# Performance work log

Hardware: AMD Instinct MI355X
Metric: run time of the kernel (lower is better)

Reference implementation:

```python
import jax, jax.numpy as jnp
import numpy as np

D_MODEL = 256
NHEAD = 8
AGG = 4
NPE = (832.0, 832.0, 832.0, 832.0)
LAYER_NAMES = ['self', 'cross'] * 4


def layer_norm(x, g, b, eps=1e-5):
    mu = x.mean(-1, keepdims=True)
    var = ((x - mu) ** 2).mean(-1, keepdims=True)
    return (x - mu) * jax.lax.rsqrt(var + eps) * g + b


def rope_tables(h, w, d_model=D_MODEL):
    # i/j positions start at 1 (torch cumsum of ones); npe train/test scaling
    i = (jnp.arange(1, h + 1, dtype=jnp.float32) * (NPE[0] / NPE[2]))[:, None, None]
    j = (jnp.arange(1, w + 1, dtype=jnp.float32) * (NPE[1] / NPE[3]))[None, :, None]
    d4 = d_model // 4
    div = jnp.exp(jnp.arange(d4, dtype=jnp.float32) * (-np.log(10000.0) / d4))

    def interleave(a, bb):
        a = jnp.broadcast_to(a, (h, w, d4))
        bb = jnp.broadcast_to(bb, (h, w, d4))
        return jnp.stack([a, bb], -1).reshape(h, w, 2 * d4)

    sin = interleave(jnp.sin(i * div), jnp.sin(j * div))
    cos = interleave(jnp.cos(i * div), jnp.cos(j * div))
    return jnp.repeat(sin, 2, axis=-1), jnp.repeat(cos, 2, axis=-1)  # [h,w,d_model]


def rotate_half(x):
    xp = x.reshape(*x.shape[:-1], -1, 2)
    return jnp.stack([-xp[..., 1], xp[..., 0]], -1).reshape(*x.shape)


def apply_rope(x, sin, cos):  # x: [b,h,w,c]
    return x * cos + rotate_half(x) * sin


def encoder_layer(x, source, p, use_rope):
    bs, C, H0, W0 = x.shape
    # depthwise-conv aggregation of query features (stride=kernel=AGG, no bias)
    q = jax.lax.conv_general_dilated(
        x, p['agg_w'], (AGG, AGG), 'VALID',
        dimension_numbers=('NCHW', 'OIHW', 'NCHW'), feature_group_count=C)
    q = layer_norm(q.transpose(0, 2, 3, 1), p['ln1_g'], p['ln1_b'])  # [b,h,w,C]
    # max-pool aggregation of source features
    s = jax.lax.reduce_window(source, -jnp.inf, jax.lax.max,
                              (1, 1, AGG, AGG), (1, 1, AGG, AGG), 'VALID')
    s = layer_norm(s.transpose(0, 2, 3, 1), p['ln1_g'], p['ln1_b'])
    query = q @ p['qw']
    key = s @ p['kw']
    value = s @ p['vw']
    if use_rope:
        sin_q, cos_q = rope_tables(query.shape[1], query.shape[2])
        query = apply_rope(query, sin_q, cos_q)
        sin_k, cos_k = rope_tables(key.shape[1], key.shape[2])
        key = apply_rope(key, sin_k, cos_k)
    L = query.shape[1] * query.shape[2]
    S = key.shape[1] * key.shape[2]
    dh = C // NHEAD
    qh = query.reshape(bs, L, NHEAD, dh)
    kh = key.reshape(bs, S, NHEAD, dh)
    vh = value.reshape(bs, S, NHEAD, dh)
    scores = jnp.einsum('blhd,bshd->bhls', qh, kh) / jnp.asarray(dh, qh.dtype) ** 0.5
    attn = jax.nn.softmax(scores, axis=-1)
    m = jnp.einsum('bhls,bshd->blhd', attn, vh).reshape(bs, L, C)
    m = m @ p['mw']  # merge
    m = m.reshape(bs, H0 // AGG, W0 // AGG, C).transpose(0, 3, 1, 2)
    # bilinear upsample x4, align_corners=False (half-pixel, matches jax.image)
    m = jax.image.resize(m, (bs, C, H0, W0), method='bilinear')
    cat = jnp.concatenate([x, m], axis=1).transpose(0, 2, 3, 1)  # [b,H,W,2C]
    h1 = cat @ p['w1']
    h1 = jnp.where(h1 >= 0, h1, 0.01 * h1)  # LeakyReLU
    out = layer_norm(h1 @ p['w2'], p['ln2_g'], p['ln2_b']).transpose(0, 3, 1, 2)
    return x + out


def _forward(feat0, feat1, params):
    for i, name in enumerate(LAYER_NAMES):
        p = {k: v[i] for k, v in params.items()}
        if name == 'self':
            feat0 = encoder_layer(feat0, feat0, p, use_rope=True)
            feat1 = encoder_layer(feat1, feat1, p, use_rope=True)
        else:
            feat0 = encoder_layer(feat0, feat1, p, use_rope=False)
            feat1 = encoder_layer(feat1, feat0, p, use_rope=False)
    return feat0, feat1


def setup_inputs() -> dict:
    key = jax.random.key(0)
    ks = jax.random.split(key, 10)
    C = D_MODEL
    NL = len(LAYER_NAMES)

    def xavier(k, shape, fan_in, fan_out):
        return jax.random.normal(k, shape, jnp.float32) * np.sqrt(2.0 / (fan_in + fan_out))

    return {
        'feat0': jax.random.normal(ks[0], (2, C, 96, 96), jnp.float32),
        'feat1': jax.random.normal(ks[1], (2, C, 96, 96), jnp.float32),
        'agg_w': jax.random.normal(ks[2], (NL, C, 1, AGG, AGG), jnp.float32) * 0.1,
        'qw': xavier(ks[3], (NL, C, C), C, C),
        'kw': xavier(ks[4], (NL, C, C), C, C),
        'vw': xavier(ks[5], (NL, C, C), C, C),
        'mw': xavier(ks[6], (NL, C, C), C, C),
        'w1': xavier(ks[7], (NL, 2 * C, 2 * C), 2 * C, 2 * C),
        'w2': xavier(ks[8], (NL, 2 * C, C), 2 * C, C),
        'ln1_g': jnp.ones((NL, C), jnp.float32),
        'ln1_b': jnp.zeros((NL, C), jnp.float32),
        'ln2_g': jnp.ones((NL, C), jnp.float32),
        'ln2_b': jnp.zeros((NL, C), jnp.float32),
    }


def reference(feat0, feat1, agg_w, qw, kw, vw, mw, w1, w2, ln1_g, ln1_b, ln2_g, ln2_b):
    params = dict(agg_w=agg_w, qw=qw, kw=kw, vw=vw, mw=mw, w1=w1, w2=w2,
                  ln1_g=ln1_g, ln1_b=ln1_b, ln2_g=ln2_g, ln2_b=ln2_b)
    return _forward(feat0, feat1, params)
```

## Files before the change

kernel.cpp:

```cpp
#include <hip/hip_runtime.h>
#include <math.h>

constexpr int BSZ = 2;
constexpr int CH  = 256;
constexpr int IH  = 96, IW = 96;
constexpr int HSS = 24, WSS = 24;
constexpr int SL  = HSS * WSS;
constexpr int NHD = 8, DHD = 32;
constexpr int CH2 = 512;
constexpr int PIX = IH * IW;
constexpr int MFFN = BSZ * PIX;
constexpr long FEATN = (long)BSZ * PIX * CH;

typedef __attribute__((ext_vector_type(4))) float f32x4;
typedef _Float16 f16;
typedef __attribute__((ext_vector_type(8))) _Float16 f16x8;
typedef __attribute__((ext_vector_type(4))) _Float16 f16x4;


__device__ inline void gload16(const void* g, void* l) {
  __builtin_amdgcn_global_load_lds(
      (const __attribute__((address_space(1))) unsigned int*)g,
      (__attribute__((address_space(3))) unsigned int*)l, 16, 0, 0);
}

__global__ __launch_bounds__(256) void k_in_tr(const float* __restrict__ in,
                                               f16* __restrict__ outh) {
  __shared__ float t[32][33];
  const int b = blockIdx.z;
  const int p0 = blockIdx.x * 32, c0 = blockIdx.y * 32;
  const int tx = threadIdx.x & 31, ty = threadIdx.x >> 5;
#pragma unroll
  for (int r = 0; r < 4; ++r)
    t[tx][ty + r * 8] = in[((long)b * CH + c0 + ty + r * 8) * PIX + p0 + tx];
  __syncthreads();
#pragma unroll
  for (int r = 0; r < 4; ++r) {
    long row = (long)b * PIX + p0 + ty + r * 8;
    outh[row * CH + ((c0 + tx) ^ (ty << 3))] = (f16)t[ty + r * 8][tx];
  }
}

__global__ __launch_bounds__(256) void k_out_tr(const f16* __restrict__ in,
                                                float* __restrict__ out) {
  __shared__ float t[32][33];
  const int b = blockIdx.z;
  const int p0 = blockIdx.x * 32, c0 = blockIdx.y * 32;
  const int tx = threadIdx.x & 31, ty = threadIdx.x >> 5;
#pragma unroll
  for (int r = 0; r < 4; ++r)
    t[ty + r * 8][tx] =
        (float)in[((long)b * PIX + p0 + ty + r * 8) * CH + ((c0 + tx) ^ (ty << 3))];
  __syncthreads();
#pragma unroll
  for (int r = 0; r < 4; ++r)
    out[((long)b * CH + c0 + ty + r * 8) * PIX + p0 + tx] = t[tx][ty + r * 8];
}

__global__ __launch_bounds__(256) void k_wt(const float* __restrict__ W,
                                            f16* __restrict__ WT,
                                            int K, int N, long strideW, long strideT) {
  const long z = blockIdx.z;
  W  += z * strideW;
  WT += z * strideT;
  __shared__ float t[32][33];
  const int n0 = blockIdx.x * 32, k0 = blockIdx.y * 32;
  const int tx = threadIdx.x & 31, ty = threadIdx.x >> 5;
#pragma unroll
  for (int r = 0; r < 4; ++r)
    t[ty + r * 8][tx] = W[(long)(k0 + ty + r * 8) * N + n0 + tx];
  __syncthreads();
#pragma unroll
  for (int r = 0; r < 4; ++r) {
    int n = n0 + ty + r * 8;
    WT[(long)n * K + ((k0 + tx) ^ ((n & 7) << 3))] = (f16)t[tx][ty + r * 8];
  }
}

__global__ __launch_bounds__(256) void k_cvt(const float* __restrict__ W,
                                             f16* __restrict__ O) {
  const int i = blockIdx.x;
  const long z = blockIdx.y;
  const int k = threadIdx.x;
  O[(z * CH + i) * CH + (k ^ ((i & 7) << 3))] = (f16)W[(z * CH + i) * CH + k];
}

__global__ __launch_bounds__(256) void k_rope_tables(float* __restrict__ sinT,
                                                     float* __restrict__ cosT) {
  int l = blockIdx.x;
  int d = threadIdx.x;
  int ii = l / WSS + 1;
  int jj = l % WSS + 1;
  int kidx = d >> 2;
  bool is_i = ((d >> 1) & 1) == 0;
  float div = expf((float)kidx * -0.14391156831212787f);
  float pos = is_i ? (float)ii : (float)jj;
  float ang = pos * div;
  sinT[(long)l * CH + d] = sinf(ang);
  cosT[(long)l * CH + d] = cosf(ang);
}

__global__ __launch_bounds__(64) void k_agg(const f16* __restrict__ x,
                                            const f16* __restrict__ src,
                                            const float* __restrict__ aggw,
                                            const float* __restrict__ g,
                                            const float* __restrict__ bt,
                                            f16* __restrict__ qln,
                                            f16* __restrict__ sln,
                                            int nb, int same) {
  int bi = blockIdx.x;
  int mode = 0;
  const int nblk = nb * SL / 2;
  if (!same && bi >= nblk) { mode = 1; bi -= nblk; }
  const int doConv = same || (mode == 0);
  const int doPool = same || (mode == 1);
  const int tid = threadIdx.x;
  const int tok = tid >> 5, cg = tid & 31;
  const int lg = bi * 2 + tok;
  const int b = lg / SL, l = lg - b * SL;
  const int i = l / WSS, j = l - i * WSS;
  const f16* in = mode ? src : x;

  float cv[8] = {};
  float mv[8];
#pragma unroll
  for (int e = 0; e < 8; ++e) mv[e] = -INFINITY;
#pragma unroll
  for (int r = 0; r < 4; ++r)
#pragma unroll
    for (int s = 0; s < 4; ++s) {
      const int px = j * 4 + s;
      f16x8 v = *(const f16x8*)&in[(((size_t)b * IH + i * 4 + r) * IW + px) * CH +
                                   ((cg * 8) ^ ((px & 7) << 3))];
#pragma unroll
      for (int e = 0; e < 8; ++e) {
        float f = (float)v[e];
        cv[e] += f * aggw[(cg * 8 + e) * 16 + r * 4 + s];
        mv[e] = fmaxf(mv[e], f);
      }
    }
  const size_t orow = (size_t)(b * SL + l) * CH + ((cg * 8) ^ ((l & 7) << 3));
  if (doConv) {
    float s1 = 0.f, s2 = 0.f;
#pragma unroll
    for (int e = 0; e < 8; ++e) { s1 += cv[e]; s2 += cv[e] * cv[e]; }
#pragma unroll
    for (int d = 1; d < 32; d <<= 1) { s1 += __shfl_xor(s1, d); s2 += __shfl_xor(s2, d); }
    float mu = s1 * (1.f / CH);
    float var = s2 * (1.f / CH) - mu * mu;
    float rs = rsqrtf(var + 1e-5f);
    f16x8 o;
#pragma unroll
    for (int e = 0; e < 8; ++e)
      o[e] = (f16)((cv[e] - mu) * rs * g[cg * 8 + e] + bt[cg * 8 + e]);
    *(f16x8*)&qln[orow] = o;
  }
  if (doPool) {
    float s1 = 0.f, s2 = 0.f;
#pragma unroll
    for (int e = 0; e < 8; ++e) { s1 += mv[e]; s2 += mv[e] * mv[e]; }
#pragma unroll
    for (int d = 1; d < 32; d <<= 1) { s1 += __shfl_xor(s1, d); s2 += __shfl_xor(s2, d); }
    float mu = s1 * (1.f / CH);
    float var = s2 * (1.f / CH) - mu * mu;
    float rs = rsqrtf(var + 1e-5f);
    f16x8 o;
#pragma unroll
    for (int e = 0; e < 8; ++e)
      o[e] = (f16)((mv[e] - mu) * rs * g[cg * 8 + e] + bt[cg * 8 + e]);
    *(f16x8*)&sln[orow] = o;
  }
}

template <int BM, int BN, int OUT>
__global__ __launch_bounds__(256) void k_mm(const f16* __restrict__ A,
                                            const f16* __restrict__ A2,
                                            const f16* __restrict__ Bt,
                                            void* __restrict__ C0, void* __restrict__ C1,
                                            void* __restrict__ C2,
                                            int M, int K, int lda, int ldb,
                                            int koffA, int koffB, int ldc,
                                            const float* __restrict__ sinT,
                                            const float* __restrict__ cosT,
                                            long zsA, long zsB, long zsC) {
  constexpr int BK = 64;
  constexpr int WM = BM / 2, WN = BN / 2;
  constexpr int FM = WM / 16, FN = WN / 16;
  constexpr int RA = BM * BK / 2048, RB = BN * BK / 2048;
  __shared__ f16 As[2][BM * BK];
  __shared__ f16 Bs[2][BN * BK];
  const int tid = threadIdx.x;
  const int lane = tid & 63, w = tid >> 6;
  const int wr = w >> 1, wc = w & 1;
  const int lq = lane & 15, g = lane >> 4;
  const int sw = (lq & 7) << 3;
  const int bm = blockIdx.x * BM, bn = blockIdx.y * BN;
  const long z = blockIdx.z;
  const f16* Ap = ((OUT == 4 && bn >= CH) ? A2 : A) + z * zsA + koffA;
  const f16* Bp = Bt + z * zsB + koffB;

  auto stA = [&](int buf, int k0) {
#pragma unroll
    for (int i = 0; i < RA; ++i) {
      int e = (i * 256 + tid) * 8;
      gload16(Ap + (size_t)(bm + (e >> 6)) * lda + k0 + (e & 63), &As[buf][e]);
    }
  };
  auto stB = [&](int buf, int k0) {
#pragma unroll
    for (int i = 0; i < RB; ++i) {
      int e = (i * 256 + tid) * 8;
      gload16(Bp + (size_t)(bn + (e >> 6)) * ldb + k0 + (e & 63), &Bs[buf][e]);
    }
  };

  f32x4 acc[FM][FN] = {};
  stA(0, 0); stB(0, 0);
  asm volatile("s_waitcnt vmcnt(0)" ::: "memory");
  __syncthreads();
  int cur = 0;
  for (int k0 = 0; k0 < K; k0 += BK) {
    if (k0 + BK < K) { stA(cur ^ 1, k0 + BK); stB(cur ^ 1, k0 + BK); }
#pragma unroll
    for (int ks = 0; ks < 2; ++ks) {
      const int kx = (ks * 32 + g * 8) ^ sw;
      f16x8 a[FM], b[FN];
#pragma unroll
      for (int m = 0; m < FM; ++m)
        a[m] = *(const f16x8*)&As[cur][(wr * WM + m * 16 + lq) * BK + kx];
#pragma unroll
      for (int n = 0; n < FN; ++n)
        b[n] = *(const f16x8*)&Bs[cur][(wc * WN + n * 16 + lq) * BK + kx];
#pragma unroll
      for (int m = 0; m < FM; ++m)
#pragma unroll
        for (int n = 0; n < FN; ++n)
          acc[m][n] = __builtin_amdgcn_mfma_f32_16x16x32_f16(a[m], b[n], acc[m][n], 0, 0, 0);
    }
    __syncthreads();
    cur ^= 1;
  }
#pragma unroll
  for (int m = 0; m < FM; ++m) {
    const int rowb = bm + wr * WM + m * 16 + g * 4;
#pragma unroll
    for (int n = 0; n < FN; ++n) {
      const int col = bn + wc * WN + n * 16 + lq;
#pragma unroll
      for (int r = 0; r < 4; ++r) {
        const int row = rowb + r;
        float v = acc[m][n][r];
        if (OUT == 0) {
          ((float*)C0 + z * zsC)[(size_t)row * ldc + col] = v;
        } else if (OUT == 5) {
          ((f16*)C0 + z * zsC)[(size_t)row * ldc + (col ^ ((row & 7) << 3))] = (f16)v;
        } else {
          const int b = row / SL, s = row - b * SL;
          const int which = col >> 8;
          const int ch = col & 255;
          float vp = __shfl_xor(v, 1);
          if (which < 2 && sinT) {
            float sn = sinT[(size_t)s * CH + ch];
            float cs = cosT[(size_t)s * CH + ch];
            v = ((lane & 1) == 0) ? v * cs - vp * sn : v * cs + vp * sn;
          }
          if (which == 0) v *= 0.17677669529663687f;
          const int h = ch >> 5, d = ch & 31;
          if (which == 0)
            ((f16*)C0)[(((size_t)b * NHD + h) * SL + s) * DHD + d] = (f16)v;
          else if (which == 1)
            ((f16*)C1)[(((size_t)b * NHD + h) * SL + s) * DHD + d] = (f16)v;
          else
            ((f16*)C2)[(((size_t)b * NHD + h) * DHD + d) * SL + s] = (f16)v;
        }
      }
    }
  }
}

__global__ __launch_bounds__(128) void k_attn(const f16* __restrict__ qh,
                                              const f16* __restrict__ kh,
                                              const f16* __restrict__ vt,
                                              f16* __restrict__ msgA) {
  const int bh = blockIdx.x;
  const int b = bh >> 3, h = bh & 7;
  const int tid = threadIdx.x;
  const int sid = tid >> 6;
  const int lane = tid & 63;
  const int lq = lane & 15, g = lane >> 4;
  const int q0 = blockIdx.y * 16;

  const f16x8 qf = *(const f16x8*)&qh[((size_t)bh * SL + q0 + lq) * DHD + g * 8];
  const f16* kbase = kh + (size_t)bh * SL * DHD;
  const f16* vbase = vt + (size_t)bh * DHD * SL;
  const int t0 = sid * 18;

  f16x8 kf = *(const f16x8*)&kbase[((size_t)(t0 * 16 + lq)) * DHD + g * 8];
  f16x4 va = *(const f16x4*)&vbase[(size_t)lq * SL + t0 * 16 + g * 4];
  f16x4 vb = *(const f16x4*)&vbase[(size_t)(16 + lq) * SL + t0 * 16 + g * 4];

  f32x4 o0 = {}, o1 = {};
  float m = -1e30f, l = 0.f;
  for (int tt = 0; tt < 18; ++tt) {
    const int t = t0 + tt;
    const int tn = tt < 17 ? t + 1 : t;
    f16x8 kfn = *(const f16x8*)&kbase[((size_t)(tn * 16 + lq)) * DHD + g * 8];
    f16x4 van = *(const f16x4*)&vbase[(size_t)lq * SL + tn * 16 + g * 4];
    f16x4 vbn = *(const f16x4*)&vbase[(size_t)(16 + lq) * SL + tn * 16 + g * 4];
    f32x4 s = __builtin_amdgcn_mfma_f32_16x16x32_f16(kf, qf, (f32x4){0.f, 0.f, 0.f, 0.f}, 0, 0, 0);
    float tm = fmaxf(fmaxf(s[0], s[1]), fmaxf(s[2], s[3]));
    tm = fmaxf(tm, __shfl_xor(tm, 16));
    tm = fmaxf(tm, __shfl_xor(tm, 32));
    if (__any(tm > m + 5.f)) {
      float mn = fmaxf(m, tm);
      float f = __expf(m - mn);
      o0 *= f; o1 *= f; l *= f; m = mn;
    }
    float e0 = __expf(s[0] - m), e1 = __expf(s[1] - m);
    float e2 = __expf(s[2] - m), e3 = __expf(s[3] - m);
    l += (e0 + e1) + (e2 + e3);
    f16x4 ef = {(f16)e0, (f16)e1, (f16)e2, (f16)e3};
    o0 = __builtin_amdgcn_mfma_f32_16x16x16f16(va, ef, o0, 0, 0, 0);
    o1 = __builtin_amdgcn_mfma_f32_16x16x16f16(vb, ef, o1, 0, 0, 0);
    kf = kfn; va = van; vb = vbn;
  }
  l += __shfl_xor(l, 16);
  l += __shfl_xor(l, 32);

  __shared__ float mS[2][16], lS[2][16];
  __shared__ float oS[2][2][16][17];
  if (g == 0) { mS[sid][lq] = m; lS[sid][lq] = l; }
#pragma unroll
  for (int r = 0; r < 4; ++r) {
    oS[sid][0][g * 4 + r][lq] = o0[r];
    oS[sid][1][g * 4 + r][lq] = o1[r];
  }
  __syncthreads();
  float m0 = mS[0][lq], m1 = mS[1][lq];
  float l0 = lS[0][lq], l1 = lS[1][lq];
  float mn = fmaxf(m0, m1);
  float f0 = __expf(m0 - mn), f1 = __expf(m1 - mn);
  float inv = 1.f / (l0 * f0 + l1 * f1);
  f16x4 ov;
#pragma unroll
  for (int r = 0; r < 4; ++r)
    ov[r] = (f16)((oS[0][sid][g * 4 + r][lq] * f0 + oS[1][sid][g * 4 + r][lq] * f1) * inv);
  const int swz = (lq & 7) << 3;
  f16* mrow = msgA + ((size_t)(b * SL + q0 + lq)) * CH;
  *(f16x4*)&mrow[(h * DHD + sid * 16 + g * 4) ^ swz] = ov;
}

__global__ __launch_bounds__(512) void k_ffn1(const f16* __restrict__ xh,
                                              const f16* __restrict__ w1T,
                                              const float* __restrict__ Z,
                                              f16* __restrict__ h1) {
  constexpr int BM = 128, BN = 128, BK = 64, K = 256;
  constexpr int WM = 32, WN = 64, FM = 2, FN = 4;
  __shared__ f16 As[2][BM * BK];
  __shared__ f16 Bs[BN * BK];
  const int tid = threadIdx.x;
  const int lane = tid & 63, w = tid >> 6;
  const int wr = w >> 1, wc = w & 1;
  const int lq = lane & 15, g = lane >> 4;
  const int sw = (lq & 7) << 3;
  const int bm = blockIdx.x * BM, bn = blockIdx.y * BN;

  auto stA = [&](int buf, int k0) {
#pragma unroll
    for (int i = 0; i < 2; ++i) {
      int e = (i * 512 + tid) * 8;
      gload16(xh + (size_t)(bm + (e >> 6)) * 256 + k0 + (e & 63), &As[buf][e]);
    }
  };
  auto stB = [&](int k0) {
#pragma unroll
    for (int i = 0; i < 2; ++i) {
      int e = (i * 512 + tid) * 8;
      gload16(w1T + (size_t)(bn + (e >> 6)) * 512 + k0 + (e & 63), &Bs[e]);
    }
  };

  f32x4 acc[FM][FN] = {};
  stA(0, 0); stB(0);
  asm volatile("s_waitcnt vmcnt(0)" ::: "memory");
  __syncthreads();
  int cur = 0;
  for (int k0 = 0; k0 < K; k0 += BK) {
    if (k0 + BK < K) stA(cur ^ 1, k0 + BK);
#pragma unroll
    for (int ks = 0; ks < 2; ++ks) {
      const int kx = (ks * 32 + g * 8) ^ sw;
      f16x8 a[FM], b[FN];
#pragma unroll
      for (int m = 0; m < FM; ++m)
        a[m] = *(const f16x8*)&As[cur][(wr * WM + m * 16 + lq) * BK + kx];
#pragma unroll
      for (int n = 0; n < FN; ++n)
        b[n] = *(const f16x8*)&Bs[(wc * WN + n * 16 + lq) * BK + kx];
#pragma unroll
      for (int m = 0; m < FM; ++m)
#pragma unroll
        for (int n = 0; n < FN; ++n)
          acc[m][n] = __builtin_amdgcn_mfma_f32_16x16x32_f16(a[m], b[n], acc[m][n], 0, 0, 0);
    }
    __syncthreads();
    if (k0 + BK < K) stB(k0 + BK);
    asm volatile("s_waitcnt vmcnt(0)" ::: "memory");
    __syncthreads();
    cur ^= 1;
  }
#pragma unroll
  for (int m = 0; m < FM; ++m) {
    const int rowb = bm + wr * WM + m * 16 + g * 4;
#pragma unroll
    for (int r = 0; r < 4; ++r) {
      const int row = rowb + r;
      const int b = row / PIX;
      const int p = row - b * PIX;
      const int y = p / IW, xx = p - y * IW;
      float sy = (y + 0.5f) * 0.25f - 0.5f;
      float sx = (xx + 0.5f) * 0.25f - 0.5f;
      int y0 = (int)floorf(sy); float wy = sy - y0;
      int x0 = (int)floorf(sx); float wx = sx - x0;
      int y1 = min(y0 + 1, HSS - 1); y0 = max(y0, 0);
      int x1 = min(x0 + 1, WSS - 1); x0 = max(x0, 0);
      const float* Zb = Z + (size_t)b * SL * CH2;
      const float* z00 = Zb + (size_t)(y0 * WSS + x0) * CH2;
      const float* z01 = Zb + (size_t)(y0 * WSS + x1) * CH2;
      const float* z10 = Zb + (size_t)(y1 * WSS + x0) * CH2;
      const float* z11 = Zb + (size_t)(y1 * WSS + x1) * CH2;
      float w00 = (1.f - wy) * (1.f - wx), w01 = (1.f - wy) * wx;
      float w10 = wy * (1.f - wx), w11 = wy * wx;
      const int rs = (row & 7) << 3;
#pragma unroll
      for (int n = 0; n < FN; ++n) {
        const int col = bn + wc * WN + n * 16 + lq;
        float v = acc[m][n][r] + w00 * z00[col] + w01 * z01[col] +
                  w10 * z10[col] + w11 * z11[col];
        v = v >= 0.f ? v : 0.01f * v;
        h1[(size_t)row * CH2 + (col ^ rs)] = (f16)v;
      }
    }
  }
}

__global__ __launch_bounds__(512) void k_ffn2(const f16* __restrict__ A,
                                              const f16* __restrict__ Bt,
                                              const float* __restrict__ g2,
                                              const float* __restrict__ b2,
                                              f16* __restrict__ xh) {
  constexpr int BM = 64, BK = 64, K = 512;
  __shared__ f16 As[2][BM * BK];
  __shared__ f16 Bs[256 * BK];
  __shared__ float sS[2][BM], sQ[2][BM];
  __shared__ float gS[256], bS[256];
  const int tid = threadIdx.x;
  const int lane = tid & 63, w = tid >> 6;
  const int wr = w >> 1, wc = w & 1;
  const int lq = lane & 15, g = lane >> 4;
  const int sw = (lq & 7) << 3;
  const int bm = blockIdx.x * BM;
  if (tid < 256) { gS[tid] = g2[tid]; bS[tid] = b2[tid]; }

  auto stA = [&](int buf, int k0) {
    int e = tid * 8;
    gload16(A + (size_t)(bm + (e >> 6)) * K + k0 + (e & 63), &As[buf][e]);
  };
  auto stB = [&](int k0) {
#pragma unroll
    for (int i = 0; i < 4; ++i) {
      int e = (i * 512 + tid) * 8;
      gload16(Bt + (size_t)(e >> 6) * K + k0 + (e & 63), &Bs[e]);
    }
  };

  f32x4 acc[8] = {};
  stA(0, 0); stB(0);
  asm volatile("s_waitcnt vmcnt(0)" ::: "memory");
  __syncthreads();
  int cur = 0;
  for (int k0 = 0; k0 < K; k0 += BK) {
    if (k0 + BK < K) stA(cur ^ 1, k0 + BK);
#pragma unroll
    for (int ks = 0; ks < 2; ++ks) {
      const int kx = (ks * 32 + g * 8) ^ sw;
      f16x8 a = *(const f16x8*)&As[cur][(wr * 16 + lq) * BK + kx];
      f16x8 b[8];
#pragma unroll
      for (int n = 0; n < 8; ++n)
        b[n] = *(const f16x8*)&Bs[(wc * 128 + n * 16 + lq) * BK + kx];
#pragma unroll
      for (int n = 0; n < 8; ++n)
        acc[n] = __builtin_amdgcn_mfma_f32_16x16x32_f16(a, b[n], acc[n], 0, 0, 0);
    }
    __syncthreads();
    if (k0 + BK < K) stB(k0 + BK);
    asm volatile("s_waitcnt vmcnt(0)" ::: "memory");
    __syncthreads();
    cur ^= 1;
  }
#pragma unroll
  for (int r = 0; r < 4; ++r) {
    float s1 = 0.f, s2 = 0.f;
#pragma unroll
    for (int n = 0; n < 8; ++n) {
      float v = acc[n][r];
      s1 += v; s2 += v * v;
    }
#pragma unroll
    for (int d = 1; d < 16; d <<= 1) {
      s1 += __shfl_xor(s1, d);
      s2 += __shfl_xor(s2, d);
    }
    if (lq == 0) {
      int row = wr * 16 + g * 4 + r;
      sS[wc][row] = s1; sQ[wc][row] = s2;
    }
  }
  __syncthreads();
#pragma unroll
  for (int r = 0; r < 4; ++r) {
    int row = wr * 16 + g * 4 + r;
    float mu = (sS[0][row] + sS[1][row]) * (1.f / CH);
    float var = (sQ[0][row] + sQ[1][row]) * (1.f / CH) - mu * mu;
    float rs = rsqrtf(var + 1e-5f);
    f16* base = xh + (size_t)(bm + row) * CH;
    const int swr = ((bm + row) & 7) << 3;
#pragma unroll
    for (int n = 0; n < 8; ++n) {
      int col = wc * 128 + n * 16 + lq;
      float o = (acc[n][r] - mu) * rs * gS[col] + bS[col];
      int ci = col ^ swr;
      base[ci] = (f16)((float)base[ci] + o);
    }
  }
}

struct LayerP {
  const float *aggw, *g1, *b1, *g2, *b2;
  const f16 *qkvT, *w1T, *w2T, *wcT;
};

struct Bufs {
  f16 *qln, *sln, *msgA, *h1, *xh;
  f16 *qh, *kh, *vt;
  float *Zbuf;
  const float *sinT, *cosT;
};

static void attn_part(long xoff, long soff, const LayerP& p, bool rope, int nb,
                      const Bufs& B, hipStream_t stream) {
  const int M = nb * SL;
  const int same = (xoff == soff) ? 1 : 0;
  const int nblk = (same ? 1 : 2) * nb * SL / 2;
  k_agg<<<dim3(nblk), 64, 0, stream>>>(B.xh + xoff, B.xh + soff, p.aggw,
                                       p.g1, p.b1, B.qln, B.sln, nb, same);
  const float* sT = rope ? B.sinT : nullptr;
  const float* cT = rope ? B.cosT : nullptr;
  k_mm<32, 64, 4><<<dim3(M / 32, 12), 256, 0, stream>>>(
      B.qln, B.sln, p.qkvT, B.qh, B.kh, B.vt, M, CH, CH, CH, 0, 0, 0, sT, cT, 0, 0, 0);
  k_attn<<<dim3(nb * NHD, 36), 128, 0, stream>>>(B.qh, B.kh, B.vt, B.msgA);
  k_mm<64, 64, 0><<<dim3(M / 64, 8), 256, 0, stream>>>(
      B.msgA, nullptr, p.wcT, B.Zbuf, nullptr, nullptr, M, CH, CH, CH, 0, 0, CH2,
      nullptr, nullptr, 0, 0, 0);
}

static void ffn_part(int fi, int nf, const float* Zs, const LayerP& p, const Bufs& B,
                     hipStream_t stream) {
  const int M = nf * MFFN;
  k_ffn1<<<dim3(M / 128, CH2 / 128), 512, 0, stream>>>(B.xh + (long)fi * FEATN, p.w1T, Zs, B.h1);
  k_ffn2<<<dim3(M / 64), 512, 0, stream>>>(B.h1, p.w2T, p.g2, p.b2,
                                           B.xh + (long)fi * FEATN);
}

extern "C" void kernel_launch(void* const* d_in, const int* in_sizes, int n_in,
                              void* d_out, int out_size, void* d_ws, size_t ws_size,
                              hipStream_t stream) {
  const float* in_f0 = (const float*)d_in[0];
  const float* in_f1 = (const float*)d_in[1];
  const float* aggw  = (const float*)d_in[2];
  const float* qw    = (const float*)d_in[3];
  const float* kw    = (const float*)d_in[4];
  const float* vw    = (const float*)d_in[5];
  const float* mw    = (const float*)d_in[6];
  const float* w1    = (const float*)d_in[7];
  const float* w2    = (const float*)d_in[8];
  const float* g1    = (const float*)d_in[9];
  const float* b1    = (const float*)d_in[10];
  const float* g2    = (const float*)d_in[11];
  const float* b2    = (const float*)d_in[12];
  (void)in_sizes; (void)n_in; (void)out_size; (void)ws_size;

  char* cur = (char*)d_ws;
  auto alloc = [&](size_t bytes) { void* p = cur; cur += (bytes + 255) & ~(size_t)255; return p; };
  f16*   xh   = (f16*)alloc((size_t)2 * FEATN * 2);
  f16*   h1   = (f16*)alloc((size_t)2 * MFFN * CH2 * 2);
  float* Zbuf = (float*)alloc((size_t)4 * SL * CH2 * 4);
  f16*   msgA = (f16*)alloc((size_t)4 * SL * CH * 2);
  f16*   qln  = (f16*)alloc((size_t)4 * SL * CH * 2);
  f16*   sln  = (f16*)alloc((size_t)4 * SL * CH * 2);
  f16* qh = (f16*)alloc((size_t)4 * NHD * SL * DHD * 2);
  f16* kh = (f16*)alloc((size_t)4 * NHD * SL * DHD * 2);
  f16* vt = (f16*)alloc((size_t)4 * NHD * SL * DHD * 2);
  float* sinT = (float*)alloc((size_t)SL * CH * 4);
  float* cosT = (float*)alloc((size_t)SL * CH * 4);
  f16* qkvT = (f16*)alloc((size_t)8 * 3 * CH * CH * 2);
  f16* mwH  = (f16*)alloc((size_t)8 * CH * CH * 2);
  f16* w1T  = (f16*)alloc((size_t)8 * CH2 * CH2 * 2);
  f16* w2T  = (f16*)alloc((size_t)8 * CH * CH2 * 2);
  f16* wcT  = (f16*)alloc((size_t)8 * CH2 * CH * 2);

  k_in_tr<<<dim3(PIX / 32, CH / 32, BSZ), 256, 0, stream>>>(in_f0, xh);
  k_in_tr<<<dim3(PIX / 32, CH / 32, BSZ), 256, 0, stream>>>(in_f1, xh + FEATN);
  k_rope_tables<<<dim3(SL), 256, 0, stream>>>(sinT, cosT);
  k_wt<<<dim3(CH / 32, CH / 32, 8), 256, 0, stream>>>(qw, qkvT, CH, CH, (long)CH * CH, (long)3 * CH * CH);
  k_wt<<<dim3(CH / 32, CH / 32, 8), 256, 0, stream>>>(kw, qkvT + (size_t)CH * CH, CH, CH, (long)CH * CH, (long)3 * CH * CH);
  k_wt<<<dim3(CH / 32, CH / 32, 8), 256, 0, stream>>>(vw, qkvT + (size_t)2 * CH * CH, CH, CH, (long)CH * CH, (long)3 * CH * CH);
  k_cvt<<<dim3(CH, 8), 256, 0, stream>>>(mw, mwH);
  k_wt<<<dim3(CH2 / 32, CH2 / 32, 8), 256, 0, stream>>>(w1, w1T, CH2, CH2, (long)CH2 * CH2, (long)CH2 * CH2);
  k_wt<<<dim3(CH / 32, CH2 / 32, 8), 256, 0, stream>>>(w2, w2T, CH2, CH, (long)CH2 * CH, (long)CH * CH2);
  k_mm<64, 64, 5><<<dim3(CH2 / 64, CH / 64, 8), 256, 0, stream>>>(
      w1T, nullptr, mwH, wcT, nullptr, nullptr, CH2, CH, CH2, CH, 256, 0, CH,
      nullptr, nullptr, (long)CH2 * CH2, (long)CH * CH, (long)CH2 * CH);

  Bufs B{qln, sln, msgA, h1, xh, qh, kh, vt, Zbuf, sinT, cosT};

  for (int i = 0; i < 8; ++i) {
    LayerP p{aggw + (long)i * CH * 16,
             g1 + i * CH, b1 + i * CH, g2 + i * CH, b2 + i * CH,
             qkvT + (long)i * 3 * CH * CH,
             w1T + (long)i * CH2 * CH2, w2T + (long)i * CH * CH2,
             wcT + (long)i * CH2 * CH};
    if ((i & 1) == 0) {
      attn_part(0, 0, p, true, 4, B, stream);
      ffn_part(0, 2, Zbuf, p, B, stream);
    } else {
      attn_part(0, FEATN, p, false, 2, B, stream);
      ffn_part(0, 1, Zbuf, p, B, stream);
      attn_part(FEATN, 0, p, false, 2, B, stream);
      ffn_part(1, 1, Zbuf, p, B, stream);
    }
  }

  float* outp = (float*)d_out;
  k_out_tr<<<dim3(PIX / 32, CH / 32, BSZ), 256, 0, stream>>>(xh, outp);
  k_out_tr<<<dim3(PIX / 32, CH / 32, BSZ), 256, 0, stream>>>(xh + FEATN, outp + FEATN);
}
```

Baseline: 975.4 us.

## Split FFN2 into a 128x128-tiled GEMM plus a separate LayerNorm-residual kernel

The second FFN GEMM previously used a 64-row tile covering all 256 output columns so it could fuse LayerNorm and the residual add. It now reuses a templated 128x128 GEMM shared with FFN1, writing an fp16 intermediate h2, and a new lightweight kernel does the LayerNorm and residual update. The message-projection output Z is also stored in fp16 instead of fp32, halving its traffic and its reads in the FFN1 bilinear epilogue. In exchange, the fused epilogue becomes an extra launch plus an h2 write and read, and Z loses precision.

```diff
diff --git a/kernel.cpp b/kernel.cpp
--- a/kernel.cpp
+++ b/kernel.cpp
@@ -254,6 +254,8 @@
           ((float*)C0 + z * zsC)[(size_t)row * ldc + col] = v;
         } else if (OUT == 5) {
           ((f16*)C0 + z * zsC)[(size_t)row * ldc + (col ^ ((row & 7) << 3))] = (f16)v;
+        } else if (OUT == 6) {
+          ((f16*)C0 + z * zsC)[(size_t)row * ldc + col] = (f16)v;
         } else {
           const int b = row / SL, s = row - b * SL;
           const int which = col >> 8;
@@ -350,11 +352,13 @@
   *(f16x4*)&mrow[(h * DHD + sid * 16 + g * 4) ^ swz] = ov;
 }
 
-__global__ __launch_bounds__(512) void k_ffn1(const f16* __restrict__ xh,
-                                              const f16* __restrict__ w1T,
-                                              const float* __restrict__ Z,
-                                              f16* __restrict__ h1) {
-  constexpr int BM = 128, BN = 128, BK = 64, K = 256;
+template <int K, bool ZEPI>
+__global__ __launch_bounds__(512) void k_ffn(const f16* __restrict__ A,
+                                             const f16* __restrict__ Bt,
+                                             const f16* __restrict__ Z,
+                                             f16* __restrict__ C,
+                                             int lda, int ldc) {
+  constexpr int BM = 128, BN = 128, BK = 64;
   constexpr int WM = 32, WN = 64, FM = 2, FN = 4;
   __shared__ f16 As[2][BM * BK];
   __shared__ f16 Bs[BN * BK];
@@ -369,14 +373,14 @@
 #pragma unroll
     for (int i = 0; i < 2; ++i) {
       int e = (i * 512 + tid) * 8;
-      gload16(xh + (size_t)(bm + (e >> 6)) * 256 + k0 + (e & 63), &As[buf][e]);
+      gload16(A + (size_t)(bm + (e >> 6)) * lda + k0 + (e & 63), &As[buf][e]);
     }
   };
   auto stB = [&](int k0) {
 #pragma unroll
     for (int i = 0; i < 2; ++i) {
       int e = (i * 512 + tid) * 8;
-      gload16(w1T + (size_t)(bn + (e >> 6)) * 512 + k0 + (e & 63), &Bs[e]);
+      gload16(Bt + (size_t)(bn + (e >> 6)) * 512 + k0 + (e & 63), &Bs[e]);
     }
   };
 
@@ -415,125 +419,71 @@
 #pragma unroll
     for (int r = 0; r < 4; ++r) {
       const int row = rowb + r;
-      const int b = row / PIX;
-      const int p = row - b * PIX;
-      const int y = p / IW, xx = p - y * IW;
-      float sy = (y + 0.5f) * 0.25f - 0.5f;
-      float sx = (xx + 0.5f) * 0.25f - 0.5f;
-      int y0 = (int)floorf(sy); float wy = sy - y0;
-      int x0 = (int)floorf(sx); float wx = sx - x0;
-      int y1 = min(y0 + 1, HSS - 1); y0 = max(y0, 0);
-      int x1 = min(x0 + 1, WSS - 1); x0 = max(x0, 0);
-      const float* Zb = Z + (size_t)b * SL * CH2;
-      const float* z00 = Zb + (size_t)(y0 * WSS + x0) * CH2;
-      const float* z01 = Zb + (size_t)(y0 * WSS + x1) * CH2;
-      const float* z10 = Zb + (size_t)(y1 * WSS + x0) * CH2;
-      const float* z11 = Zb + (size_t)(y1 * WSS + x1) * CH2;
-      float w00 = (1.f - wy) * (1.f - wx), w01 = (1.f - wy) * wx;
-      float w10 = wy * (1.f - wx), w11 = wy * wx;
       const int rs = (row & 7) << 3;
-#pragma unroll
-      for (int n = 0; n < FN; ++n) {
-        const int col = bn + wc * WN + n * 16 + lq;
-        float v = acc[m][n][r] + w00 * z00[col] + w01 * z01[col] +
-                  w10 * z10[col] + w11 * z11[col];
-        v = v >= 0.f ? v : 0.01f * v;
-        h1[(size_t)row * CH2 + (col ^ rs)] = (f16)v;
+      if (ZEPI) {
+        const int b = row / PIX;
+        const int p = row - b * PIX;
+        const int y = p / IW, xx = p - y * IW;
+        float sy = (y + 0.5f) * 0.25f - 0.5f;
+        float sx = (xx + 0.5f) * 0.25f - 0.5f;
+        int y0 = (int)floorf(sy); float wy = sy - y0;
+        int x0 = (int)floorf(sx); float wx = sx - x0;
+        int y1 = min(y0 + 1, HSS - 1); y0 = max(y0, 0);
+        int x1 = min(x0 + 1, WSS - 1); x0 = max(x0, 0);
+        const f16* Zb = Z + (size_t)b * SL * CH2;
+        const f16* z00 = Zb + (size_t)(y0 * WSS + x0) * CH2;
+        const f16* z01 = Zb + (size_t)(y0 * WSS + x1) * CH2;
+        const f16* z10 = Zb + (size_t)(y1 * WSS + x0) * CH2;
+        const f16* z11 = Zb + (size_t)(y1 * WSS + x1) * CH2;
+        float w00 = (1.f - wy) * (1.f - wx), w01 = (1.f - wy) * wx;
+        float w10 = wy * (1.f - wx), w11 = wy * wx;
+#pragma unroll
+        for (int n = 0; n < FN; ++n) {
+          const int col = bn + wc * WN + n * 16 + lq;
+          float v = acc[m][n][r] + w00 * (float)z00[col] + w01 * (float)z01[col] +
+                    w10 * (float)z10[col] + w11 * (float)z11[col];
+          v = v >= 0.f ? v : 0.01f * v;
+          C[(size_t)row * ldc + (col ^ rs)] = (f16)v;
+        }
+      } else {
+#pragma unroll
+        for (int n = 0; n < FN; ++n) {
+          const int col = bn + wc * WN + n * 16 + lq;
+          C[(size_t)row * ldc + (col ^ rs)] = (f16)acc[m][n][r];
+        }
       }
     }
   }
 }
 
-__global__ __launch_bounds__(512) void k_ffn2(const f16* __restrict__ A,
-                                              const f16* __restrict__ Bt,
-                                              const float* __restrict__ g2,
-                                              const float* __restrict__ b2,
-                                              f16* __restrict__ xh) {
-  constexpr int BM = 64, BK = 64, K = 512;
-  __shared__ f16 As[2][BM * BK];
-  __shared__ f16 Bs[256 * BK];
-  __shared__ float sS[2][BM], sQ[2][BM];
+__global__ __launch_bounds__(256) void k_lnres(const f16* __restrict__ h2,
+                                               const float* __restrict__ g2,
+                                               const float* __restrict__ b2,
+                                               f16* __restrict__ xh) {
   __shared__ float gS[256], bS[256];
   const int tid = threadIdx.x;
-  const int lane = tid & 63, w = tid >> 6;
-  const int wr = w >> 1, wc = w & 1;
-  const int lq = lane & 15, g = lane >> 4;
-  const int sw = (lq & 7) << 3;
-  const int bm = blockIdx.x * BM;
-  if (tid < 256) { gS[tid] = g2[tid]; bS[tid] = b2[tid]; }
-
-  auto stA = [&](int buf, int k0) {
-    int e = tid * 8;
-    gload16(A + (size_t)(bm + (e >> 6)) * K + k0 + (e & 63), &As[buf][e]);
-  };
-  auto stB = [&](int k0) {
-#pragma unroll
-    for (int i = 0; i < 4; ++i) {
-      int e = (i * 512 + tid) * 8;
-      gload16(Bt + (size_t)(e >> 6) * K + k0 + (e & 63), &Bs[e]);
-    }
-  };
-
-  f32x4 acc[8] = {};
-  stA(0, 0); stB(0);
-  asm volatile("s_waitcnt vmcnt(0)" ::: "memory");
+  gS[tid] = g2[tid]; bS[tid] = b2[tid];
   __syncthreads();
-  int cur = 0;
-  for (int k0 = 0; k0 < K; k0 += BK) {
-    if (k0 + BK < K) stA(cur ^ 1, k0 + BK);
-#pragma unroll
-    for (int ks = 0; ks < 2; ++ks) {
-      const int kx = (ks * 32 + g * 8) ^ sw;
-      f16x8 a = *(const f16x8*)&As[cur][(wr * 16 + lq) * BK + kx];
-      f16x8 b[8];
-#pragma unroll
-      for (int n = 0; n < 8; ++n)
-        b[n] = *(const f16x8*)&Bs[(wc * 128 + n * 16 + lq) * BK + kx];
-#pragma unroll
-      for (int n = 0; n < 8; ++n)
-        acc[n] = __builtin_amdgcn_mfma_f32_16x16x32_f16(a, b[n], acc[n], 0, 0, 0);
-    }
-    __syncthreads();
-    if (k0 + BK < K) stB(k0 + BK);
-    asm volatile("s_waitcnt vmcnt(0)" ::: "memory");
-    __syncthreads();
-    cur ^= 1;
-  }
-#pragma unroll
-  for (int r = 0; r < 4; ++r) {
-    float s1 = 0.f, s2 = 0.f;
-#pragma unroll
-    for (int n = 0; n < 8; ++n) {
-      float v = acc[n][r];
-      s1 += v; s2 += v * v;
-    }
-#pragma unroll
-    for (int d = 1; d < 16; d <<= 1) {
-      s1 += __shfl_xor(s1, d);
-      s2 += __shfl_xor(s2, d);
-    }
-    if (lq == 0) {
-      int row = wr * 16 + g * 4 + r;
-      sS[wc][row] = s1; sQ[wc][row] = s2;
-    }
-  }
-  __syncthreads();
-#pragma unroll
-  for (int r = 0; r < 4; ++r) {
-    int row = wr * 16 + g * 4 + r;
-    float mu = (sS[0][row] + sS[1][row]) * (1.f / CH);
-    float var = (sQ[0][row] + sQ[1][row]) * (1.f / CH) - mu * mu;
-    float rs = rsqrtf(var + 1e-5f);
-    f16* base = xh + (size_t)(bm + row) * CH;
-    const int swr = ((bm + row) & 7) << 3;
-#pragma unroll
-    for (int n = 0; n < 8; ++n) {
-      int col = wc * 128 + n * 16 + lq;
-      float o = (acc[n][r] - mu) * rs * gS[col] + bS[col];
-      int ci = col ^ swr;
-      base[ci] = (f16)((float)base[ci] + o);
-    }
-  }
+  const int row = blockIdx.x * 8 + (tid >> 5);
+  const int c = tid & 31;
+  const int swr = (row & 7) << 3;
+  const size_t off = (size_t)row * CH + ((c * 8) ^ swr);
+  f16x8 v = *(const f16x8*)&h2[off];
+  float s1 = 0.f, s2 = 0.f;
+  float f[8];
+#pragma unroll
+  for (int e = 0; e < 8; ++e) { f[e] = (float)v[e]; s1 += f[e]; s2 += f[e] * f[e]; }
+#pragma unroll
+  for (int d = 1; d < 32; d <<= 1) { s1 += __shfl_xor(s1, d); s2 += __shfl_xor(s2, d); }
+  float mu = s1 * (1.f / CH);
+  float var = s2 * (1.f / CH) - mu * mu;
+  float rs = rsqrtf(var + 1e-5f);
+  f16x8 x = *(const f16x8*)&xh[off];
+  f16x8 o;
+#pragma unroll
+  for (int e = 0; e < 8; ++e)
+    o[e] = (f16)((float)x[e] + (f[e] - mu) * rs * gS[c * 8 + e] + bS[c * 8 + e]);
+  *(f16x8*)&xh[off] = o;
 }
 
 struct LayerP {
@@ -542,9 +492,9 @@
 };
 
 struct Bufs {
-  f16 *qln, *sln, *msgA, *h1, *xh;
+  f16 *qln, *sln, *msgA, *h1, *h2, *xh;
   f16 *qh, *kh, *vt;
-  float *Zbuf;
+  f16 *Zbuf;
   const float *sinT, *cosT;
 };
 
@@ -560,17 +510,19 @@
   k_mm<32, 64, 4><<<dim3(M / 32, 12), 256, 0, stream>>>(
       B.qln, B.sln, p.qkvT, B.qh, B.kh, B.vt, M, CH, CH, CH, 0, 0, 0, sT, cT, 0, 0, 0);
   k_attn<<<dim3(nb * NHD, 36), 128, 0, stream>>>(B.qh, B.kh, B.vt, B.msgA);
-  k_mm<64, 64, 0><<<dim3(M / 64, 8), 256, 0, stream>>>(
+  k_mm<64, 64, 6><<<dim3(M / 64, 8), 256, 0, stream>>>(
       B.msgA, nullptr, p.wcT, B.Zbuf, nullptr, nullptr, M, CH, CH, CH, 0, 0, CH2,
       nullptr, nullptr, 0, 0, 0);
 }
 
-static void ffn_part(int fi, int nf, const float* Zs, const LayerP& p, const Bufs& B,
+static void ffn_part(int fi, int nf, const f16* Zs, const LayerP& p, const Bufs& B,
                      hipStream_t stream) {
   const int M = nf * MFFN;
-  k_ffn1<<<dim3(M / 128, CH2 / 128), 512, 0, stream>>>(B.xh + (long)fi * FEATN, p.w1T, Zs, B.h1);
-  k_ffn2<<<dim3(M / 64), 512, 0, stream>>>(B.h1, p.w2T, p.g2, p.b2,
-                                           B.xh + (long)fi * FEATN);
+  k_ffn<256, true><<<dim3(M / 128, CH2 / 128), 512, 0, stream>>>(
+      B.xh + (long)fi * FEATN, p.w1T, Zs, B.h1, CH, CH2);
+  k_ffn<512, false><<<dim3(M / 128, CH / 128), 512, 0, stream>>>(
+      B.h1, p.w2T, nullptr, B.h2, CH2, CH);
+  k_lnres<<<dim3(M / 8), 256, 0, stream>>>(B.h2, p.g2, p.b2, B.xh + (long)fi * FEATN);
 }
 
 extern "C" void kernel_launch(void* const* d_in, const int* in_sizes, int n_in,
@@ -595,7 +547,8 @@
   auto alloc = [&](size_t bytes) { void* p = cur; cur += (bytes + 255) & ~(size_t)255; return p; };
   f16*   xh   = (f16*)alloc((size_t)2 * FEATN * 2);
   f16*   h1   = (f16*)alloc((size_t)2 * MFFN * CH2 * 2);
-  float* Zbuf = (float*)alloc((size_t)4 * SL * CH2 * 4);
+  f16*   h2   = (f16*)alloc((size_t)2 * MFFN * CH * 2);
+  f16*   Zbuf = (f16*)alloc((size_t)4 * SL * CH2 * 2);
   f16*   msgA = (f16*)alloc((size_t)4 * SL * CH * 2);
   f16*   qln  = (f16*)alloc((size_t)4 * SL * CH * 2);
   f16*   sln  = (f16*)alloc((size_t)4 * SL * CH * 2);
@@ -623,7 +576,7 @@
       w1T, nullptr, mwH, wcT, nullptr, nullptr, CH2, CH, CH2, CH, 256, 0, CH,
       nullptr, nullptr, (long)CH2 * CH2, (long)CH * CH, (long)CH2 * CH);
 
-  Bufs B{qln, sln, msgA, h1, xh, qh, kh, vt, Zbuf, sinT, cosT};
+  Bufs B{qln, sln, msgA, h1, h2, xh, qh, kh, vt, Zbuf, sinT, cosT};
 
   for (int i = 0; i < 8; ++i) {
     LayerP p{aggw + (long)i * CH * 16,
```

Measured after the change: 962.6 us. About the same (-1.3%).
